# Performance work log

Hardware: AMD Instinct MI355X
Metric: run time of the kernel (lower is better)

## Reference

```python
import jax, jax.numpy as jnp
import numpy as np

TOTAL_INSTANCES = 131072
NUM_BAGS = 64
FEATURE_DIM = 512
HIDDEN_DIM = 256


def setup_inputs() -> dict:
    key = jax.random.key(0)
    k1, k2, k3 = jax.random.split(key, 3)
    instance_features = jax.random.normal(k1, (TOTAL_INSTANCES, FEATURE_DIM), dtype=jnp.float32)
    # Equal-sized bags (sum(bag_sizes) == TOTAL_INSTANCES); the reference handles ragged sizes too.
    bag_sizes = jnp.full((NUM_BAGS,), TOTAL_INSTANCES // NUM_BAGS, dtype=jnp.int32)
    W1 = jax.random.normal(k2, (FEATURE_DIM, HIDDEN_DIM), dtype=jnp.float32) * (1.0 / np.sqrt(FEATURE_DIM))
    b1 = jnp.zeros((HIDDEN_DIM,), dtype=jnp.float32)
    W2 = jax.random.normal(k3, (HIDDEN_DIM, 1), dtype=jnp.float32) * (1.0 / np.sqrt(HIDDEN_DIM))
    b2 = jnp.zeros((1,), dtype=jnp.float32)
    return {
        "instance_features": instance_features,
        "bag_sizes": bag_sizes,
        "W1": W1,
        "b1": b1,
        "W2": W2,
        "b2": b2,
    }


def reference(instance_features, bag_sizes, W1, b1, W2, b2):
    # Attention MLP: Linear -> Tanh -> Linear  => scores [T, 1]
    scores = jnp.tanh(instance_features @ W1 + b1) @ W2 + b2
    # Faithful to the original: softmax over dim=0 GLOBALLY across all instances.
    weights = jax.nn.softmax(scores, axis=0)  # [T, 1]
    T = instance_features.shape[0]
    B = bag_sizes.shape[0]
    # Ragged bag membership: instance i belongs to the first bag whose cumulative
    # size exceeds i.
    offsets = jnp.cumsum(bag_sizes)  # [B]
    seg_ids = jnp.searchsorted(offsets, jnp.arange(T), side="right")  # [T]
    # Per-bag weighted sum of instances: [B, feature_dim]
    return jax.ops.segment_sum(instance_features * weights, seg_ids, num_segments=B)
```

## Files before the change

### kernel.cpp

```cpp
#include <hip/hip_runtime.h>
#include <hip/hip_bf16.h>

typedef __attribute__((ext_vector_type(8))) short short8;
typedef __attribute__((ext_vector_type(4))) float floatx4;

#define FDIM 512
#define HDIM 256

__device__ __forceinline__ unsigned short f2bf(float f) {
  unsigned int u = __float_as_uint(f);
  u += 0x7fffu + ((u >> 16) & 1u);
  return (unsigned short)(u >> 16);
}

__device__ __forceinline__ short8 pack2(float4 a, float4 b) {
  short8 r;
  r[0] = (short)f2bf(a.x); r[1] = (short)f2bf(a.y);
  r[2] = (short)f2bf(a.z); r[3] = (short)f2bf(a.w);
  r[4] = (short)f2bf(b.x); r[5] = (short)f2bf(b.y);
  r[6] = (short)f2bf(b.z); r[7] = (short)f2bf(b.w);
  return r;
}

__device__ __forceinline__ float fast_tanh(float x) {
  x = fminf(15.0f, fmaxf(-15.0f, x));
  float e = __expf(2.0f * x);
  return (e - 1.0f) / (e + 1.0f);
}

__device__ __forceinline__ void gload_lds16(const void* g, void* l) {
  __builtin_amdgcn_global_load_lds(
      (const __attribute__((address_space(1))) unsigned int*)g,
      (__attribute__((address_space(3))) unsigned int*)l, 16, 0, 0);
}

__global__ void __launch_bounds__(256)
k0_pack_w1(const float* __restrict__ W1, unsigned short* __restrict__ W1B,
           float* __restrict__ out) {
  int tid = threadIdx.x;
  int idx = blockIdx.x * 256 + tid;
  if (blockIdx.x < 128) out[blockIdx.x * 256 + tid] = 0.0f;
  int k = idx >> 8;
  int n = idx & 255;
  int s = k >> 5, r = k & 31, oct = r >> 3, e = r & 7;
  W1B[s * 8192 + oct * 2048 + n * 8 + e] = f2bf(W1[idx]);
}

__global__ void __launch_bounds__(512)
k1_scores(const float* __restrict__ X,
          const unsigned short* __restrict__ W1B,
          const float* __restrict__ b1,
          const float* __restrict__ W2,
          float* __restrict__ es,
          float* __restrict__ partials) {
  __shared__ __align__(16) unsigned short As[8192];
  __shared__ __align__(16) unsigned short Bs[16384];
  __shared__ float scpart[4][128];
  __shared__ float wsum_s[2];

  const int tid  = threadIdx.x;
  const int wid  = tid >> 6;
  const int lane = tid & 63;
  const int l15  = lane & 15;
  const int l4   = lane >> 4;
  const int wr   = wid >> 2;
  const int wn   = wid & 3;
  const long row0 = (long)blockIdx.x * 128;

  floatx4 acc[4][4];
  #pragma unroll
  for (int m = 0; m < 4; m++)
    #pragma unroll
    for (int n = 0; n < 4; n++)
      acc[m][n] = (floatx4){0.f, 0.f, 0.f, 0.f};

  const int arow = tid >> 2;
  const int akc  = (tid & 3) * 16;
  const float* xsrc = X + (row0 + arow) * FDIM + akc;
  unsigned short* adst = As + ((akc >> 3) * 128 + arow) * 8;

  float4 v0, v1, v2, v3;
  { const float4* p = (const float4*)xsrc; v0 = p[0]; v1 = p[1]; v2 = p[2]; v3 = p[3]; }

  for (int t = 0; t < 8; ++t) {
    short8 a01 = pack2(v0, v1);
    short8 a23 = pack2(v2, v3);
    __syncthreads();
    *(short8*)adst          = a01;
    *(short8*)(adst + 1024) = a23;
    #pragma unroll
    for (int i = 0; i < 4; ++i) {
      int c = i * 512 + tid;
      gload_lds16(W1B + t * 16384 + c * 8, Bs + (i * 512 + wid * 64) * 8);
    }
    __syncthreads();
    if (t < 7) {
      const float4* p = (const float4*)(xsrc + (t + 1) * 64);
      v0 = p[0]; v1 = p[1]; v2 = p[2]; v3 = p[3];
    }
    #pragma unroll
    for (int ks = 0; ks < 2; ++ks) {
      short8 af[4];
      #pragma unroll
      for (int m = 0; m < 4; ++m)
        af[m] = *(const short8*)(As + ((ks * 4 + l4) * 128 + wr * 64 + m * 16 + l15) * 8);
      #pragma unroll
      for (int n = 0; n < 4; ++n) {
        short8 bfr = *(const short8*)(Bs + ((ks * 4 + l4) * 256 + wn * 64 + n * 16 + l15) * 8);
        #pragma unroll
        for (int m = 0; m < 4; ++m)
          acc[m][n] = __builtin_amdgcn_mfma_f32_16x16x32_bf16(af[m], bfr, acc[m][n], 0, 0, 0);
      }
    }
  }

  float rowacc[16];
  #pragma unroll
  for (int i = 0; i < 16; i++) rowacc[i] = 0.f;
  #pragma unroll
  for (int n = 0; n < 4; n++) {
    int c = wn * 64 + n * 16 + l15;
    float b1c = b1[c];
    float w2c = W2[c];
    #pragma unroll
    for (int m = 0; m < 4; m++)
      #pragma unroll
      for (int j = 0; j < 4; j++) {
        float h = fast_tanh(acc[m][n][j] + b1c);
        rowacc[m * 4 + j] = fmaf(h, w2c, rowacc[m * 4 + j]);
      }
  }
  #pragma unroll
  for (int i = 0; i < 16; i++) {
    float v = rowacc[i];
    v += __shfl_xor(v, 1, 64);
    v += __shfl_xor(v, 2, 64);
    v += __shfl_xor(v, 4, 64);
    v += __shfl_xor(v, 8, 64);
    rowacc[i] = v;
  }
  if (l15 == 0) {
    #pragma unroll
    for (int m = 0; m < 4; m++)
      #pragma unroll
      for (int j = 0; j < 4; j++)
        scpart[wn][wr * 64 + m * 16 + l4 * 4 + j] = rowacc[m * 4 + j];
  }
  __syncthreads();

  if (tid < 128) {
    float sv = scpart[0][tid] + scpart[1][tid] + scpart[2][tid] + scpart[3][tid];
    float ev = __expf(sv);
    es[row0 + tid] = ev;
    float v = ev;
    v += __shfl_xor(v, 1, 64);
    v += __shfl_xor(v, 2, 64);
    v += __shfl_xor(v, 4, 64);
    v += __shfl_xor(v, 8, 64);
    v += __shfl_xor(v, 16, 64);
    v += __shfl_xor(v, 32, 64);
    if (lane == 0) wsum_s[wid] = v;
  }
  __syncthreads();
  if (tid == 0) partials[blockIdx.x] = wsum_s[0] + wsum_s[1];
}

__global__ void __launch_bounds__(256)
k2b_finish(const float* __restrict__ partials, int nparts, float* __restrict__ invZ) {
  int tid = threadIdx.x;
  float s = 0.f;
  for (int j = tid; j < nparts; j += 256) s += partials[j];
  #pragma unroll
  for (int m = 1; m < 64; m <<= 1) s += __shfl_xor(s, m, 64);
  __shared__ float wred[4];
  if ((tid & 63) == 0) wred[tid >> 6] = s;
  __syncthreads();
  if (tid == 0) invZ[0] = 1.0f / (wred[0] + wred[1] + wred[2] + wred[3]);
}

__global__ void __launch_bounds__(256)
k3_bagsum(const float* __restrict__ X, const int* __restrict__ bag_sizes,
          const float* __restrict__ es, const float* __restrict__ invZp,
          float* __restrict__ out, int nbags) {
  const int tid = threadIdx.x;
  const int f   = (tid & 127) * 4;
  const int r   = tid >> 7;
  const int bag = blockIdx.x >> 4;
  const int ic  = blockIdx.x & 15;
  int start = 0;
  for (int b = 0; b < bag; ++b) start += bag_sizes[b];
  const int size = bag_sizes[bag];
  const int end = start + size;
  const int chunk = (size + 15) >> 4;
  int i0 = start + ic * chunk;
  int i1 = min(i0 + chunk, end);
  float ax = 0.f, ay = 0.f, az = 0.f, aw = 0.f;
  for (int i = i0 + r; i < i1; i += 2) {
    float w = es[i];
    float4 x = *(const float4*)(X + (size_t)i * FDIM + f);
    ax = fmaf(x.x, w, ax); ay = fmaf(x.y, w, ay);
    az = fmaf(x.z, w, az); aw = fmaf(x.w, w, aw);
  }
  __shared__ float4 red[128];
  if (r == 1) red[tid & 127] = (float4){ax, ay, az, aw};
  __syncthreads();
  if (r == 0) {
    float4 o = red[tid];
    float invZ = invZp[0];
    ax = (ax + o.x) * invZ; ay = (ay + o.y) * invZ;
    az = (az + o.z) * invZ; aw = (aw + o.w) * invZ;
    float* op = out + (size_t)bag * FDIM + f;
    atomicAdd(op + 0, ax); atomicAdd(op + 1, ay);
    atomicAdd(op + 2, az); atomicAdd(op + 3, aw);
  }
}

extern "C" void kernel_launch(void* const* d_in, const int* in_sizes, int n_in,
                              void* d_out, int out_size, void* d_ws, size_t ws_size,
                              hipStream_t stream) {
  const float* X         = (const float*)d_in[0];
  const int*   bag_sizes = (const int*)d_in[1];
  const float* W1        = (const float*)d_in[2];
  const float* b1        = (const float*)d_in[3];
  const float* W2        = (const float*)d_in[4];
  float* out = (float*)d_out;

  const int T     = in_sizes[0] / FDIM;
  const int nbags = in_sizes[1];
  const int nblk  = T / 128;

  char* ws = (char*)d_ws;
  unsigned short* W1B = (unsigned short*)ws;
  float* es       = (float*)(ws + 262144);
  float* partials = (float*)(ws + 262144 + 524288);
  float* invZ     = (float*)(ws + 262144 + 524288 + 4096);

  hipLaunchKernelGGL(k0_pack_w1, dim3(512), dim3(256), 0, stream, W1, W1B, out);
  hipLaunchKernelGGL(k1_scores, dim3(nblk), dim3(512), 0, stream,
                     X, W1B, b1, W2, es, partials);
  hipLaunchKernelGGL(k2b_finish, dim3(1), dim3(256), 0, stream, partials, nblk, invZ);
  hipLaunchKernelGGL(k3_bagsum, dim3(nbags * 16), dim3(256), 0, stream,
                     X, bag_sizes, es, invZ, out, nbags);
}
```

Measured before the change: 118.0 us.

## Fuse bag weighted-sum into score kernel using LDS-resident bf16 X tile

The score kernel now keeps the whole 128x512 bf16 X tile in a 128KB XOR-swizzled LDS buffer and double-buffers W1 in 16-wide K steps. After computing the exp scores it does the per-bag weighted sum directly from LDS and atomically adds unnormalized results to the output. A final small kernel rescales the output by 1/Z. This removes the second full read of X from HBM and drops two launches. In exchange, occupancy falls to one block per CU because of the large LDS use, and the bag sums now use bf16-rounded X, which lowers precision.

```diff
diff --git a/kernel.cpp b/kernel.cpp
--- a/kernel.cpp
+++ b/kernel.cpp
@@ -1,5 +1,4 @@
 #include <hip/hip_runtime.h>
-#include <hip/hip_bf16.h>
 
 typedef __attribute__((ext_vector_type(8))) short short8;
 typedef __attribute__((ext_vector_type(4))) float floatx4;
@@ -47,16 +46,21 @@
 }
 
 __global__ void __launch_bounds__(512)
-k1_scores(const float* __restrict__ X,
-          const unsigned short* __restrict__ W1B,
-          const float* __restrict__ b1,
-          const float* __restrict__ W2,
-          float* __restrict__ es,
-          float* __restrict__ partials) {
-  __shared__ __align__(16) unsigned short As[8192];
-  __shared__ __align__(16) unsigned short Bs[16384];
-  __shared__ float scpart[4][128];
-  __shared__ float wsum_s[2];
+k1_fused(const float* __restrict__ X,
+         const unsigned short* __restrict__ W1B,
+         const float* __restrict__ b1,
+         const float* __restrict__ W2,
+         const int* __restrict__ bag_sizes,
+         int nbags,
+         float* __restrict__ out,
+         float* __restrict__ partials) {
+  __shared__ __align__(16) unsigned char smem[163840];
+  unsigned short* As  = (unsigned short*)smem;
+  unsigned short* Bs0 = (unsigned short*)(smem + 131072);
+  unsigned short* Bs1 = (unsigned short*)(smem + 147456);
+  float* scpart = (float*)(smem + 131072);
+  float* es_s   = (float*)(smem + 131072 + 2048);
+  float* wsum_s = (float*)(smem + 131072 + 2560);
 
   const int tid  = threadIdx.x;
   const int wid  = tid >> 6;
@@ -75,42 +79,49 @@
       acc[m][n] = (floatx4){0.f, 0.f, 0.f, 0.f};
 
   const int arow = tid >> 2;
-  const int akc  = (tid & 3) * 16;
-  const float* xsrc = X + (row0 + arow) * FDIM + akc;
-  unsigned short* adst = As + ((akc >> 3) * 128 + arow) * 8;
-
-  float4 v0, v1, v2, v3;
-  { const float4* p = (const float4*)xsrc; v0 = p[0]; v1 = p[1]; v2 = p[2]; v3 = p[3]; }
-
-  for (int t = 0; t < 8; ++t) {
-    short8 a01 = pack2(v0, v1);
-    short8 a23 = pack2(v2, v3);
+  const int aoct = tid & 3;
+  const float* xsrc = X + (row0 + arow) * FDIM + aoct * 8;
+
+  float4 va0, va1, vb0, vb1;
+  { const float4* pp = (const float4*)xsrc;        va0 = pp[0]; va1 = pp[1]; }
+  { const float4* pp = (const float4*)(xsrc + 32); vb0 = pp[0]; vb1 = pp[1]; }
+  #pragma unroll
+  for (int i = 0; i < 2; ++i)
+    gload_lds16(W1B + (i * 512 + tid) * 8, Bs0 + (i * 512 + wid * 64) * 8);
+
+  for (int t = 0; t < 16; ++t) {
+    unsigned short* Bcur = (t & 1) ? Bs1 : Bs0;
+    {
+      int slot = t * 4 + aoct;
+      unsigned short* dst = As + (slot * 128 + (arow ^ (slot & 7))) * 8;
+      if ((t & 1) == 0) *(short8*)dst = pack2(va0, va1);
+      else              *(short8*)dst = pack2(vb0, vb1);
+    }
     __syncthreads();
-    *(short8*)adst          = a01;
-    *(short8*)(adst + 1024) = a23;
-    #pragma unroll
-    for (int i = 0; i < 4; ++i) {
-      int c = i * 512 + tid;
-      gload_lds16(W1B + t * 16384 + c * 8, Bs + (i * 512 + wid * 64) * 8);
-    }
-    __syncthreads();
-    if (t < 7) {
-      const float4* p = (const float4*)(xsrc + (t + 1) * 64);
-      v0 = p[0]; v1 = p[1]; v2 = p[2]; v3 = p[3];
-    }
-    #pragma unroll
-    for (int ks = 0; ks < 2; ++ks) {
-      short8 af[4];
+    if (t < 14) {
+      const float4* pp = (const float4*)(xsrc + (t + 2) * 32);
+      if ((t & 1) == 0) { va0 = pp[0]; va1 = pp[1]; }
+      else              { vb0 = pp[0]; vb1 = pp[1]; }
+    }
+    if (t < 15) {
+      unsigned short* Bn = (t & 1) ? Bs0 : Bs1;
+      #pragma unroll
+      for (int i = 0; i < 2; ++i)
+        gload_lds16(W1B + (t + 1) * 8192 + (i * 512 + tid) * 8,
+                    Bn + (i * 512 + wid * 64) * 8);
+    }
+    const int slotc = t * 4 + l4;
+    const int gg = slotc & 7;
+    short8 af[4];
+    #pragma unroll
+    for (int m = 0; m < 4; ++m)
+      af[m] = *(const short8*)(As + (slotc * 128 + ((wr * 64 + m * 16 + l15) ^ gg)) * 8);
+    #pragma unroll
+    for (int n = 0; n < 4; ++n) {
+      short8 bfr = *(const short8*)(Bcur + (l4 * 256 + wn * 64 + n * 16 + l15) * 8);
       #pragma unroll
       for (int m = 0; m < 4; ++m)
-        af[m] = *(const short8*)(As + ((ks * 4 + l4) * 128 + wr * 64 + m * 16 + l15) * 8);
-      #pragma unroll
-      for (int n = 0; n < 4; ++n) {
-        short8 bfr = *(const short8*)(Bs + ((ks * 4 + l4) * 256 + wn * 64 + n * 16 + l15) * 8);
-        #pragma unroll
-        for (int m = 0; m < 4; ++m)
-          acc[m][n] = __builtin_amdgcn_mfma_f32_16x16x32_bf16(af[m], bfr, acc[m][n], 0, 0, 0);
-      }
+        acc[m][n] = __builtin_amdgcn_mfma_f32_16x16x32_bf16(af[m], bfr, acc[m][n], 0, 0, 0);
     }
   }
 
@@ -144,14 +155,15 @@
     for (int m = 0; m < 4; m++)
       #pragma unroll
       for (int j = 0; j < 4; j++)
-        scpart[wn][wr * 64 + m * 16 + l4 * 4 + j] = rowacc[m * 4 + j];
+        scpart[wn * 128 + wr * 64 + m * 16 + l4 * 4 + j] = rowacc[m * 4 + j];
   }
   __syncthreads();
 
   if (tid < 128) {
-    float sv = scpart[0][tid] + scpart[1][tid] + scpart[2][tid] + scpart[3][tid];
+    float sv = scpart[0 * 128 + tid] + scpart[1 * 128 + tid] +
+               scpart[2 * 128 + tid] + scpart[3 * 128 + tid];
     float ev = __expf(sv);
-    es[row0 + tid] = ev;
+    es_s[tid] = ev;
     float v = ev;
     v += __shfl_xor(v, 1, 64);
     v += __shfl_xor(v, 2, 64);
@@ -163,56 +175,74 @@
   }
   __syncthreads();
   if (tid == 0) partials[blockIdx.x] = wsum_s[0] + wsum_s[1];
+
+  const int s  = tid >> 3;
+  const int p  = tid & 7;
+  const int gp = s & 7;
+  const int fbase = (s >> 2) * 32 + (s & 3) * 8;
+  const unsigned short* abase = As + s * 1024;
+
+  int bag = 0; long cum = 0;
+  while (bag + 1 < nbags && cum + (long)bag_sizes[bag] <= row0) {
+    cum += bag_sizes[bag]; ++bag;
+  }
+  long bagEnd = cum + (long)bag_sizes[bag];
+
+  int rs = 0;
+  while (rs < 128) {
+    int se = (int)(bagEnd - row0 < 128 ? bagEnd - row0 : 128);
+    float pa[8];
+    #pragma unroll
+    for (int e = 0; e < 8; ++e) pa[e] = 0.f;
+    #pragma unroll
+    for (int j = 0; j < 16; ++j) {
+      int r = p + 8 * j;
+      if (r >= rs && r < se) {
+        float w = es_s[r];
+        short8 xv = *(const short8*)(abase + ((r ^ gp) * 8));
+        const unsigned int* ui = (const unsigned int*)&xv;
+        #pragma unroll
+        for (int d = 0; d < 4; ++d) {
+          float xlo = __uint_as_float(ui[d] << 16);
+          float xhi = __uint_as_float(ui[d] & 0xffff0000u);
+          pa[2 * d]     = fmaf(xlo, w, pa[2 * d]);
+          pa[2 * d + 1] = fmaf(xhi, w, pa[2 * d + 1]);
+        }
+      }
+    }
+    #pragma unroll
+    for (int e = 0; e < 8; ++e) {
+      pa[e] += __shfl_xor(pa[e], 1, 64);
+      pa[e] += __shfl_xor(pa[e], 2, 64);
+      pa[e] += __shfl_xor(pa[e], 4, 64);
+    }
+    if (p == 0 && se > rs) {
+      float* op = out + (long)bag * FDIM + fbase;
+      #pragma unroll
+      for (int e = 0; e < 8; ++e) atomicAdd(op + e, pa[e]);
+    }
+    rs = se;
+    if (rs < 128) {
+      ++bag;
+      if (bag >= nbags) { bagEnd = row0 + 128; bag = nbags - 1; }
+      else bagEnd += (long)bag_sizes[bag];
+    }
+  }
 }
 
 __global__ void __launch_bounds__(256)
-k2b_finish(const float* __restrict__ partials, int nparts, float* __restrict__ invZ) {
+k2_scale(const float* __restrict__ partials, int nparts, float* __restrict__ out) {
+  __shared__ float wred[4];
   int tid = threadIdx.x;
-  float s = 0.f;
-  for (int j = tid; j < nparts; j += 256) s += partials[j];
-  #pragma unroll
-  for (int m = 1; m < 64; m <<= 1) s += __shfl_xor(s, m, 64);
-  __shared__ float wred[4];
-  if ((tid & 63) == 0) wred[tid >> 6] = s;
+  float sL = 0.f;
+  for (int j = tid; j < nparts; j += 256) sL += partials[j];
+  #pragma unroll
+  for (int m = 1; m < 64; m <<= 1) sL += __shfl_xor(sL, m, 64);
+  if ((tid & 63) == 0) wred[tid >> 6] = sL;
   __syncthreads();
-  if (tid == 0) invZ[0] = 1.0f / (wred[0] + wred[1] + wred[2] + wred[3]);
-}
-
-__global__ void __launch_bounds__(256)
-k3_bagsum(const float* __restrict__ X, const int* __restrict__ bag_sizes,
-          const float* __restrict__ es, const float* __restrict__ invZp,
-          float* __restrict__ out, int nbags) {
-  const int tid = threadIdx.x;
-  const int f   = (tid & 127) * 4;
-  const int r   = tid >> 7;
-  const int bag = blockIdx.x >> 4;
-  const int ic  = blockIdx.x & 15;
-  int start = 0;
-  for (int b = 0; b < bag; ++b) start += bag_sizes[b];
-  const int size = bag_sizes[bag];
-  const int end = start + size;
-  const int chunk = (size + 15) >> 4;
-  int i0 = start + ic * chunk;
-  int i1 = min(i0 + chunk, end);
-  float ax = 0.f, ay = 0.f, az = 0.f, aw = 0.f;
-  for (int i = i0 + r; i < i1; i += 2) {
-    float w = es[i];
-    float4 x = *(const float4*)(X + (size_t)i * FDIM + f);
-    ax = fmaf(x.x, w, ax); ay = fmaf(x.y, w, ay);
-    az = fmaf(x.z, w, az); aw = fmaf(x.w, w, aw);
-  }
-  __shared__ float4 red[128];
-  if (r == 1) red[tid & 127] = (float4){ax, ay, az, aw};
-  __syncthreads();
-  if (r == 0) {
-    float4 o = red[tid];
-    float invZ = invZp[0];
-    ax = (ax + o.x) * invZ; ay = (ay + o.y) * invZ;
-    az = (az + o.z) * invZ; aw = (aw + o.w) * invZ;
-    float* op = out + (size_t)bag * FDIM + f;
-    atomicAdd(op + 0, ax); atomicAdd(op + 1, ay);
-    atomicAdd(op + 2, az); atomicAdd(op + 3, aw);
-  }
+  float invZ = 1.0f / (wred[0] + wred[1] + wred[2] + wred[3]);
+  int i = blockIdx.x * 256 + tid;
+  out[i] = out[i] * invZ;
 }
 
 extern "C" void kernel_launch(void* const* d_in, const int* in_sizes, int n_in,
@@ -231,14 +261,11 @@
 
   char* ws = (char*)d_ws;
   unsigned short* W1B = (unsigned short*)ws;
-  float* es       = (float*)(ws + 262144);
-  float* partials = (float*)(ws + 262144 + 524288);
-  float* invZ     = (float*)(ws + 262144 + 524288 + 4096);
+  float* partials = (float*)(ws + 262144);
 
   hipLaunchKernelGGL(k0_pack_w1, dim3(512), dim3(256), 0, stream, W1, W1B, out);
-  hipLaunchKernelGGL(k1_scores, dim3(nblk), dim3(512), 0, stream,
-                     X, W1B, b1, W2, es, partials);
-  hipLaunchKernelGGL(k2b_finish, dim3(1), dim3(256), 0, stream, partials, nblk, invZ);
-  hipLaunchKernelGGL(k3_bagsum, dim3(nbags * 16), dim3(256), 0, stream,
-                     X, bag_sizes, es, invZ, out, nbags);
-}
+  hipLaunchKernelGGL(k1_fused, dim3(nblk), dim3(512), 0, stream,
+                     X, W1B, b1, W2, bag_sizes, nbags, out, partials);
+  hipLaunchKernelGGL(k2_scale, dim3((nbags * FDIM) / 256), dim3(256), 0, stream,
+                     partials, nblk, out);
+}
```

New measurement: 119.0 us. Within noise of the previous version (+0.9%).

## Restructure score GEMM: B fragments in registers, double-buffered A, 64-row tiles

Applied to the files above, without the earlier changes.

The score kernel now uses 64-row tiles with 256 threads. Each wave loads its W1 bf16 fragments straight from global memory into registers through inline-asm dwordx4 loads instead of staging them in LDS. A is double-buffered in a small LDS ring with manual vmcnt waits, so one barrier per K-step replaces two. The aim is to cut LDS traffic and barrier stalls and to overlap global loads with MFMA. The cost is hand-written waitcnt bookkeeping that must stay exactly right, plus more global loads of W1 per block.

```diff
diff --git a/kernel.cpp b/kernel.cpp
--- a/kernel.cpp
+++ b/kernel.cpp
@@ -1,5 +1,4 @@
 #include <hip/hip_runtime.h>
-#include <hip/hip_bf16.h>
 
 typedef __attribute__((ext_vector_type(8))) short short8;
 typedef __attribute__((ext_vector_type(4))) float floatx4;
@@ -13,12 +12,12 @@
   return (unsigned short)(u >> 16);
 }
 
-__device__ __forceinline__ short8 pack2(float4 a, float4 b) {
+__device__ __forceinline__ short8 pack2(floatx4 a, floatx4 b) {
   short8 r;
-  r[0] = (short)f2bf(a.x); r[1] = (short)f2bf(a.y);
-  r[2] = (short)f2bf(a.z); r[3] = (short)f2bf(a.w);
-  r[4] = (short)f2bf(b.x); r[5] = (short)f2bf(b.y);
-  r[6] = (short)f2bf(b.z); r[7] = (short)f2bf(b.w);
+  r[0] = (short)f2bf(a[0]); r[1] = (short)f2bf(a[1]);
+  r[2] = (short)f2bf(a[2]); r[3] = (short)f2bf(a[3]);
+  r[4] = (short)f2bf(b[0]); r[5] = (short)f2bf(b[1]);
+  r[6] = (short)f2bf(b[2]); r[7] = (short)f2bf(b[3]);
   return r;
 }
 
@@ -28,11 +27,25 @@
   return (e - 1.0f) / (e + 1.0f);
 }
 
-__device__ __forceinline__ void gload_lds16(const void* g, void* l) {
-  __builtin_amdgcn_global_load_lds(
-      (const __attribute__((address_space(1))) unsigned int*)g,
-      (__attribute__((address_space(3))) unsigned int*)l, 16, 0, 0);
-}
+#define GLOAD_A(r0, r1, p)                                                     \
+  do {                                                                         \
+    asm volatile("global_load_dwordx4 %0, %1, off"                             \
+                 : "=v"(r0) : "v"(p) : "memory");                              \
+    asm volatile("global_load_dwordx4 %0, %1, off offset:16"                   \
+                 : "=v"(r1) : "v"(p) : "memory");                              \
+  } while (0)
+
+#define GLOAD_B(r, p)                                                          \
+  do {                                                                         \
+    asm volatile("global_load_dwordx4 %0, %1, off"                             \
+                 : "=v"(r[0]) : "v"(p) : "memory");                            \
+    asm volatile("global_load_dwordx4 %0, %1, off offset:256"                  \
+                 : "=v"(r[1]) : "v"(p) : "memory");                            \
+    asm volatile("global_load_dwordx4 %0, %1, off offset:512"                  \
+                 : "=v"(r[2]) : "v"(p) : "memory");                            \
+    asm volatile("global_load_dwordx4 %0, %1, off offset:768"                  \
+                 : "=v"(r[3]) : "v"(p) : "memory");                            \
+  } while (0)
 
 __global__ void __launch_bounds__(256)
 k0_pack_w1(const float* __restrict__ W1, unsigned short* __restrict__ W1B,
@@ -46,26 +59,22 @@
   W1B[s * 8192 + oct * 2048 + n * 8 + e] = f2bf(W1[idx]);
 }
 
-__global__ void __launch_bounds__(512)
+__global__ void __launch_bounds__(256, 2)
 k1_scores(const float* __restrict__ X,
           const unsigned short* __restrict__ W1B,
           const float* __restrict__ b1,
           const float* __restrict__ W2,
           float* __restrict__ es,
           float* __restrict__ partials) {
-  __shared__ __align__(16) unsigned short As[8192];
-  __shared__ __align__(16) unsigned short Bs[16384];
-  __shared__ float scpart[4][128];
-  __shared__ float wsum_s[2];
+  __shared__ __align__(16) unsigned short As[2][2048];
+  __shared__ float scpart[256];
 
   const int tid  = threadIdx.x;
-  const int wid  = tid >> 6;
+  const int wn   = tid >> 6;
   const int lane = tid & 63;
   const int l15  = lane & 15;
   const int l4   = lane >> 4;
-  const int wr   = wid >> 2;
-  const int wn   = wid & 3;
-  const long row0 = (long)blockIdx.x * 128;
+  const long row0 = (long)blockIdx.x * 64;
 
   floatx4 acc[4][4];
   #pragma unroll
@@ -75,43 +84,53 @@
       acc[m][n] = (floatx4){0.f, 0.f, 0.f, 0.f};
 
   const int arow = tid >> 2;
-  const int akc  = (tid & 3) * 16;
-  const float* xsrc = X + (row0 + arow) * FDIM + akc;
-  unsigned short* adst = As + ((akc >> 3) * 128 + arow) * 8;
-
-  float4 v0, v1, v2, v3;
-  { const float4* p = (const float4*)xsrc; v0 = p[0]; v1 = p[1]; v2 = p[2]; v3 = p[3]; }
-
-  for (int t = 0; t < 8; ++t) {
-    short8 a01 = pack2(v0, v1);
-    short8 a23 = pack2(v2, v3);
-    __syncthreads();
-    *(short8*)adst          = a01;
-    *(short8*)(adst + 1024) = a23;
-    #pragma unroll
-    for (int i = 0; i < 4; ++i) {
-      int c = i * 512 + tid;
-      gload_lds16(W1B + t * 16384 + c * 8, Bs + (i * 512 + wid * 64) * 8);
+  const int aoct = tid & 3;
+  const float* xsrc = X + (row0 + arow) * FDIM + aoct * 8;
+  const unsigned short* bsrc = W1B + l4 * 2048 + (wn * 64 + l15) * 8;
+
+  floatx4 va0, va1, vb0, vb1;
+  short8 br0[4], br1[4];
+
+  GLOAD_A(va0, va1, xsrc);
+  GLOAD_B(br0, bsrc);
+  GLOAD_A(vb0, vb1, xsrc + 32);
+
+  #pragma unroll
+  for (int t = 0; t < 16; ++t) {
+    if (t < 15) asm volatile("s_waitcnt vmcnt(6)" ::: "memory");
+    else        asm volatile("s_waitcnt vmcnt(4)" ::: "memory");
+    __builtin_amdgcn_sched_barrier(0);
+    {
+      short8 a = ((t & 1) == 0) ? pack2(va0, va1) : pack2(vb0, vb1);
+      *(short8*)(&As[t & 1][arow * 32 + aoct * 8]) = a;
     }
-    __syncthreads();
-    if (t < 7) {
-      const float4* p = (const float4*)(xsrc + (t + 1) * 64);
-      v0 = p[0]; v1 = p[1]; v2 = p[2]; v3 = p[3];
+    asm volatile("s_waitcnt lgkmcnt(0)" ::: "memory");
+    __builtin_amdgcn_sched_barrier(0);
+    __builtin_amdgcn_s_barrier();
+    if (t < 15) {
+      const unsigned short* bp = bsrc + (t + 1) * 8192;
+      if (((t + 1) & 1) == 0) GLOAD_B(br0, bp);
+      else                    GLOAD_B(br1, bp);
     }
-    #pragma unroll
-    for (int ks = 0; ks < 2; ++ks) {
-      short8 af[4];
+    if (t < 14) {
+      const float* pp = xsrc + (t + 2) * 32;
+      if ((t & 1) == 0) GLOAD_A(va0, va1, pp);
+      else              GLOAD_A(vb0, vb1, pp);
+    }
+    if (t < 14)       asm volatile("s_waitcnt vmcnt(8)" ::: "memory");
+    else if (t == 14) asm volatile("s_waitcnt vmcnt(6)" ::: "memory");
+    else              asm volatile("s_waitcnt vmcnt(0)" ::: "memory");
+    __builtin_amdgcn_sched_barrier(0);
+    short8 af[4];
+    #pragma unroll
+    for (int m = 0; m < 4; ++m)
+      af[m] = *(const short8*)(&As[t & 1][(m * 16 + l15) * 32 + l4 * 8]);
+    const short8* bcur = ((t & 1) == 0) ? br0 : br1;
+    #pragma unroll
+    for (int n = 0; n < 4; ++n)
       #pragma unroll
       for (int m = 0; m < 4; ++m)
-        af[m] = *(const short8*)(As + ((ks * 4 + l4) * 128 + wr * 64 + m * 16 + l15) * 8);
-      #pragma unroll
-      for (int n = 0; n < 4; ++n) {
-        short8 bfr = *(const short8*)(Bs + ((ks * 4 + l4) * 256 + wn * 64 + n * 16 + l15) * 8);
-        #pragma unroll
-        for (int m = 0; m < 4; ++m)
-          acc[m][n] = __builtin_amdgcn_mfma_f32_16x16x32_bf16(af[m], bfr, acc[m][n], 0, 0, 0);
-      }
-    }
+        acc[m][n] = __builtin_amdgcn_mfma_f32_16x16x32_bf16(af[m], bcur[n], acc[m][n], 0, 0, 0);
   }
 
   float rowacc[16];
@@ -144,12 +163,13 @@
     for (int m = 0; m < 4; m++)
       #pragma unroll
       for (int j = 0; j < 4; j++)
-        scpart[wn][wr * 64 + m * 16 + l4 * 4 + j] = rowacc[m * 4 + j];
+        scpart[wn * 64 + m * 16 + l4 * 4 + j] = rowacc[m * 4 + j];
   }
   __syncthreads();
 
-  if (tid < 128) {
-    float sv = scpart[0][tid] + scpart[1][tid] + scpart[2][tid] + scpart[3][tid];
+  if (tid < 64) {
+    float sv = scpart[0 * 64 + tid] + scpart[1 * 64 + tid] +
+               scpart[2 * 64 + tid] + scpart[3 * 64 + tid];
     float ev = __expf(sv);
     es[row0 + tid] = ev;
     float v = ev;
@@ -159,10 +179,8 @@
     v += __shfl_xor(v, 8, 64);
     v += __shfl_xor(v, 16, 64);
     v += __shfl_xor(v, 32, 64);
-    if (lane == 0) wsum_s[wid] = v;
-  }
-  __syncthreads();
-  if (tid == 0) partials[blockIdx.x] = wsum_s[0] + wsum_s[1];
+    if (tid == 0) partials[blockIdx.x] = v;
+  }
 }
 
 __global__ void __launch_bounds__(256)
@@ -227,16 +245,16 @@
 
   const int T     = in_sizes[0] / FDIM;
   const int nbags = in_sizes[1];
-  const int nblk  = T / 128;
+  const int nblk  = T / 64;
 
   char* ws = (char*)d_ws;
   unsigned short* W1B = (unsigned short*)ws;
   float* es       = (float*)(ws + 262144);
   float* partials = (float*)(ws + 262144 + 524288);
-  float* invZ     = (float*)(ws + 262144 + 524288 + 4096);
+  float* invZ     = (float*)(ws + 262144 + 524288 + 8192);
 
   hipLaunchKernelGGL(k0_pack_w1, dim3(512), dim3(256), 0, stream, W1, W1B, out);
-  hipLaunchKernelGGL(k1_scores, dim3(nblk), dim3(512), 0, stream,
+  hipLaunchKernelGGL(k1_scores, dim3(nblk), dim3(256), 0, stream,
                      X, W1B, b1, W2, es, partials);
   hipLaunchKernelGGL(k2b_finish, dim3(1), dim3(256), 0, stream, partials, nblk, invZ);
   hipLaunchKernelGGL(k3_bagsum, dim3(nbags * 16), dim3(256), 0, stream,
```

Result: faster. 107.1 us (-9.2%).
